# Kernel optimization log

Measured on AMD Instinct MI355X. Metric: run time of the kernel, lower is better.

## Reference

```python
import jax, jax.numpy as jnp
import numpy as np

N_AGENTS = 32
STATE_DIM = 512
EMBED = 64
BATCH = 32768


def setup_inputs() -> dict:
    key = jax.random.key(0)
    ks = jax.random.split(key, 16)
    g = lambda k, shape, fan_in: jax.random.normal(k, shape, jnp.float32) / np.sqrt(fan_in)
    return {
        "agent_qs": jax.random.normal(ks[0], (BATCH, N_AGENTS), jnp.float32),
        "states": jax.random.normal(ks[1], (BATCH, STATE_DIM), jnp.float32),
        # hyper_w1: Linear(state,E) -> ReLU -> Linear(E, n_agents*E)
        "w1_l1_w": g(ks[2], (EMBED, STATE_DIM), STATE_DIM),
        "w1_l1_b": jnp.zeros((EMBED,), jnp.float32),
        "w1_l2_w": g(ks[3], (N_AGENTS * EMBED, EMBED), EMBED),
        "w1_l2_b": jnp.zeros((N_AGENTS * EMBED,), jnp.float32),
        # hyper_w2: Linear(state,E) -> ReLU -> Linear(E, E)
        "w2_l1_w": g(ks[4], (EMBED, STATE_DIM), STATE_DIM),
        "w2_l1_b": jnp.zeros((EMBED,), jnp.float32),
        "w2_l2_w": g(ks[5], (EMBED, EMBED), EMBED),
        "w2_l2_b": jnp.zeros((EMBED,), jnp.float32),
        # hyper_b1: Linear(state, E)
        "b1_w": g(ks[6], (EMBED, STATE_DIM), STATE_DIM),
        "b1_b": jnp.zeros((EMBED,), jnp.float32),
        # hyper_b2: Linear(state,E) -> ReLU -> Linear(E, 1)
        "b2_l1_w": g(ks[7], (EMBED, STATE_DIM), STATE_DIM),
        "b2_l1_b": jnp.zeros((EMBED,), jnp.float32),
        "b2_l2_w": g(ks[8], (1, EMBED), EMBED),
        "b2_l2_b": jnp.zeros((1,), jnp.float32),
    }


def _linear(x, w, b):
    return x @ w.T + b


def reference(agent_qs, states,
              w1_l1_w, w1_l1_b, w1_l2_w, w1_l2_b,
              w2_l1_w, w2_l1_b, w2_l2_w, w2_l2_b,
              b1_w, b1_b, b2_l1_w, b2_l1_b, b2_l2_w, b2_l2_b):
    B = agent_qs.shape[0]
    # hypernetworks producing per-sample weights
    w1 = jnp.abs(_linear(jax.nn.relu(_linear(states, w1_l1_w, w1_l1_b)), w1_l2_w, w1_l2_b))
    w1 = w1.reshape(B, N_AGENTS, EMBED)                      # [B, A, E]
    b1 = _linear(states, b1_w, b1_b)                         # [B, E]
    hidden = jax.nn.elu(jnp.einsum('ba,bae->be', agent_qs, w1) + b1)  # [B, E]
    w2 = jnp.abs(_linear(jax.nn.relu(_linear(states, w2_l1_w, w2_l1_b)), w2_l2_w, w2_l2_b))  # [B, E]
    b2 = _linear(jax.nn.relu(_linear(states, b2_l1_w, b2_l1_b)), b2_l2_w, b2_l2_b)           # [B, 1]
    q_total = jnp.einsum('be,be->b', hidden, w2) + b2[:, 0]  # [B]
    return q_total
```

## Files before the change

### kernel.cpp

```cpp
#include <hip/hip_runtime.h>

typedef unsigned short u16;
typedef unsigned int u32;
typedef short bf16x8 __attribute__((ext_vector_type(8)));
typedef float f32x4 __attribute__((ext_vector_type(4)));

#define NAG 32
#define STATE 512
#define EMBED 64
#define TB 32

#define OFF_W1L1 0
#define OFF_W2L1 32768
#define OFF_B1W  65536
#define OFF_B2L1 98304
#define OFF_W1L2 131072
#define OFF_W2L2 262144
#define WS_TOTAL 266240

__device__ __forceinline__ float bf2f(u16 u) {
    u32 i = ((u32)u) << 16; float f;
    __builtin_memcpy(&f, &i, 4); return f;
}
__device__ __forceinline__ u16 f2bf(float f) {
    u32 i; __builtin_memcpy(&i, &f, 4);
    return (u16)((i + 0x8000u) >> 16);
}
__device__ __forceinline__ bf16x8 ld8(const u16* p) {
    return *reinterpret_cast<const bf16x8*>(p);
}
__device__ __forceinline__ bf16x8 cvt8(f32x4 a, f32x4 b) {
    bf16x8 r;
#pragma unroll
    for (int i = 0; i < 4; ++i) r[i]     = (short)f2bf(a[i]);
#pragma unroll
    for (int i = 0; i < 4; ++i) r[i + 4] = (short)f2bf(b[i]);
    return r;
}
__device__ __forceinline__ void dma16(const void* g, void* l) {
    __builtin_amdgcn_global_load_lds(
        (const __attribute__((address_space(1))) u32*)g,
        (__attribute__((address_space(3))) u32*)l, 16, 0, 0);
}

__global__ __launch_bounds__(256) void cvt_weights(
    const float* __restrict__ w1l1w, const float* __restrict__ w2l1w,
    const float* __restrict__ b1w,   const float* __restrict__ b2l1w,
    const float* __restrict__ w1l2w, const float* __restrict__ w2l2w,
    u16* __restrict__ ws)
{
    int idx = blockIdx.x * 256 + threadIdx.x;
    const float* src; int off;
    if      (idx < OFF_W2L1)  { src = w1l1w; off = OFF_W1L1; }
    else if (idx < OFF_B1W)   { src = w2l1w; off = OFF_W2L1; }
    else if (idx < OFF_B2L1)  { src = b1w;   off = OFF_B1W;  }
    else if (idx < OFF_W1L2)  { src = b2l1w; off = OFF_B2L1; }
    else if (idx < OFF_W2L2)  { src = w1l2w; off = OFF_W1L2; }
    else if (idx < WS_TOTAL)  { src = w2l2w; off = OFF_W2L2; }
    else return;
    ws[idx] = f2bf(src[idx - off]);
}

__global__ __launch_bounds__(256, 2) void qmix_kernel(
    const float* __restrict__ qs,    const float* __restrict__ st,
    const u16*  __restrict__ wsb,
    const float* __restrict__ w1l1b, const float* __restrict__ w1l2b,
    const float* __restrict__ w2l1b, const float* __restrict__ w2l2b,
    const float* __restrict__ b1b,   const float* __restrict__ b2l1b,
    const float* __restrict__ b2l2w, const float* __restrict__ b2l2b,
    float* __restrict__ out)
{
    __shared__ u16   wbuf[256 * 64];
    __shared__ float sbuf[TB * 64];
    __shared__ u16   y[TB][264];
    __shared__ u16   hid[TB][72];
    __shared__ float qsl[TB][33];
    __shared__ float w1b[2048];
    __shared__ float qacc[TB][2];
    __shared__ float b2w[64];

    const int t    = threadIdx.x;
    const int wave = t >> 6, lane = t & 63;
    const int m = lane & 15, quad = lane >> 4;
    const int sbase = blockIdx.x * TB;

    if (t < 64) b2w[t] = b2l2w[t];
    {
        int s = t >> 3, a8 = (t & 7) * 4;
        f32x4 qv = *reinterpret_cast<const f32x4*>(qs + (size_t)(sbase + s) * NAG + a8);
#pragma unroll
        for (int j = 0; j < 4; ++j) qsl[s][a8 + j] = qv[j];
    }
    {
        f32x4 a0 = *reinterpret_cast<const f32x4*>(w1l2b + t * 8);
        f32x4 a1 = *reinterpret_cast<const f32x4*>(w1l2b + t * 8 + 4);
        *reinterpret_cast<f32x4*>(&w1b[t * 8])     = a0;
        *reinterpret_cast<f32x4*>(&w1b[t * 8 + 4]) = a1;
    }

    const int shalf = wave >> 1, fhalf = wave & 1;
    const int s0 = shalf * 16;
    const int fbase = fhalf * 128;

    const float* bgA = fhalf ? b1b   : w1l1b;
    const float* bgB = fhalf ? b2l1b : w2l1b;
    float abias[8];
#pragma unroll
    for (int tt = 0; tt < 4; ++tt) abias[tt]     = bgA[tt * 16 + m];
#pragma unroll
    for (int tt = 0; tt < 4; ++tt) abias[tt + 4] = bgB[tt * 16 + m];

    f32x4 acc[8] = {};
    for (int ksl = 0; ksl < 8; ++ksl) {
        __syncthreads();
        {
            const int rsub = lane >> 3, c = lane & 7;
#pragma unroll
            for (int j = 0; j < 8; ++j) {
                const int row = wave * 64 + j * 8 + rsub;
                const int sc  = c ^ (row & 7);
                dma16(wsb + (size_t)row * STATE + ksl * 64 + sc * 8,
                      &wbuf[(wave * 64 + j * 8) * 64 + lane * 8]);
            }
        }
        {
            const int rs = lane >> 4, cs = lane & 15;
#pragma unroll
            for (int j = 0; j < 2; ++j) {
                const int row = wave * 8 + j * 4 + rs;
                const int sc  = cs ^ (row & 15);
                dma16(st + (size_t)(sbase + row) * STATE + ksl * 64 + sc * 4,
                      &sbuf[(wave * 8 + j * 4) * 64 + lane * 4]);
            }
        }
        __builtin_amdgcn_s_waitcnt(0);
        __syncthreads();
#pragma unroll
        for (int ks = 0; ks < 2; ++ks) {
            const int arow = s0 + m;
            const int gc = ks * 8 + quad * 2;
            f32x4 a0 = *reinterpret_cast<const f32x4*>(&sbuf[arow * 64 + ((gc    ) ^ (arow & 15)) * 4]);
            f32x4 a1 = *reinterpret_cast<const f32x4*>(&sbuf[arow * 64 + ((gc + 1) ^ (arow & 15)) * 4]);
            bf16x8 af = cvt8(a0, a1);
#pragma unroll
            for (int tt = 0; tt < 8; ++tt) {
                const int brow = fbase + tt * 16 + m;
                bf16x8 bf = ld8(&wbuf[brow * 64 + ((ks * 4 + quad) ^ (brow & 7)) * 8]);
                acc[tt] = __builtin_amdgcn_mfma_f32_16x16x32_bf16(af, bf, acc[tt], 0, 0, 0);
            }
        }
    }
#pragma unroll
    for (int tt = 0; tt < 8; ++tt) {
        const bool isrelu = (fhalf == 0) || (tt >= 4);
        const int fcol = fbase + tt * 16 + m;
#pragma unroll
        for (int r = 0; r < 4; ++r) {
            float v = acc[tt][r] + abias[tt];
            if (isrelu) v = fmaxf(v, 0.f);
            y[s0 + quad * 4 + r][fcol] = f2bf(v);
        }
    }
    __syncthreads();

    const int e0 = (wave & 1) * 32;
    bf16x8 haf0 = *reinterpret_cast<const bf16x8*>(&y[s0 + m][quad * 8]);
    bf16x8 haf1 = *reinterpret_cast<const bf16x8*>(&y[s0 + m][32 + quad * 8]);

    f32x4 hacc[2] = {};
    for (int bs = 0; bs < 8; ++bs) {
        {
            const int rsub = lane >> 3, c = lane & 7;
#pragma unroll
            for (int j = 0; j < 8; ++j) {
                const int row = wave * 64 + j * 8 + rsub;
                const int sc  = c ^ (row & 7);
                dma16(wsb + OFF_W1L2 + ((size_t)bs * 256 + row) * EMBED + sc * 8,
                      &wbuf[(wave * 64 + j * 8) * 64 + lane * 8]);
            }
        }
        __builtin_amdgcn_s_waitcnt(0);
        __syncthreads();
#pragma unroll
        for (int aloc = 0; aloc < 4; ++aloc) {
            const int a = bs * 4 + aloc;
            float qv[4];
#pragma unroll
            for (int r = 0; r < 4; ++r) qv[r] = qsl[s0 + quad * 4 + r][a];
#pragma unroll
            for (int tp = 0; tp < 2; ++tp) {
                const int row = aloc * 64 + e0 + tp * 16 + m;
                bf16x8 b0 = ld8(&wbuf[row * 64 + ((    quad) ^ (row & 7)) * 8]);
                bf16x8 b1 = ld8(&wbuf[row * 64 + ((4 + quad) ^ (row & 7)) * 8]);
                f32x4 p = {};
                p = __builtin_amdgcn_mfma_f32_16x16x32_bf16(haf0, b0, p, 0, 0, 0);
                p = __builtin_amdgcn_mfma_f32_16x16x32_bf16(haf1, b1, p, 0, 0, 0);
                float bias = w1b[a * EMBED + e0 + tp * 16 + m];
#pragma unroll
                for (int r = 0; r < 4; ++r)
                    hacc[tp][r] += qv[r] * fabsf(p[r] + bias);
            }
        }
        __syncthreads();
    }
#pragma unroll
    for (int tp = 0; tp < 2; ++tp) {
#pragma unroll
        for (int r = 0; r < 4; ++r) {
            int s = s0 + quad * 4 + r, e = e0 + tp * 16 + m;
            float v = hacc[tp][r] + bf2f(y[s][128 + e]);
            v = (v > 0.f) ? v : (__expf(v) - 1.f);
            hid[s][e] = f2bf(v);
        }
    }
    __syncthreads();

    bf16x8 h2f0 = *reinterpret_cast<const bf16x8*>(&y[s0 + m][64 + quad * 8]);
    bf16x8 h2f1 = *reinterpret_cast<const bf16x8*>(&y[s0 + m][64 + 32 + quad * 8]);

    const u16* wc0 = wsb + OFF_W2L2 + (size_t)((wave & 1) * 32 + m) * EMBED + quad * 8;
    f32x4 qp = {};
#pragma unroll
    for (int tp = 0; tp < 2; ++tp) {
        const int etile = (wave & 1) * 2 + tp;
        bf16x8 b0 = ld8(wc0 + tp * 1024);
        bf16x8 b1 = ld8(wc0 + tp * 1024 + 32);
        f32x4 p = {};
        p = __builtin_amdgcn_mfma_f32_16x16x32_bf16(h2f0, b0, p, 0, 0, 0);
        p = __builtin_amdgcn_mfma_f32_16x16x32_bf16(h2f1, b1, p, 0, 0, 0);
        float bias = w2l2b[etile * 16 + m];
#pragma unroll
        for (int r = 0; r < 4; ++r) {
            float w2v = fabsf(p[r] + bias);
            float hv = bf2f(hid[s0 + quad * 4 + r][etile * 16 + m]);
            qp[r] += hv * w2v;
        }
    }
#pragma unroll
    for (int off = 1; off < 16; off <<= 1) {
#pragma unroll
        for (int r = 0; r < 4; ++r) qp[r] += __shfl_xor(qp[r], off, 64);
    }
    if (m == 0) {
#pragma unroll
        for (int r = 0; r < 4; ++r) qacc[s0 + quad * 4 + r][wave & 1] = qp[r];
    }
    __syncthreads();

    if (t < TB) {
        int s = t;
        float q = qacc[s][0] + qacc[s][1] + b2l2b[0];
        float acc2 = 0.f;
#pragma unroll
        for (int kk = 0; kk < 8; ++kk) {
            bf16x8 hv = *reinterpret_cast<const bf16x8*>(&y[s][192 + kk * 8]);
#pragma unroll
            for (int j = 0; j < 8; ++j)
                acc2 += bf2f((u16)hv[j]) * b2w[kk * 8 + j];
        }
        out[sbase + s] = q + acc2;
    }
}

extern "C" void kernel_launch(void* const* d_in, const int* in_sizes, int n_in,
                              void* d_out, int out_size, void* d_ws, size_t ws_size,
                              hipStream_t stream)
{
    const float* qs    = (const float*)d_in[0];
    const float* st    = (const float*)d_in[1];
    const float* w1l1w = (const float*)d_in[2];
    const float* w1l1b = (const float*)d_in[3];
    const float* w1l2w = (const float*)d_in[4];
    const float* w1l2b = (const float*)d_in[5];
    const float* w2l1w = (const float*)d_in[6];
    const float* w2l1b = (const float*)d_in[7];
    const float* w2l2w = (const float*)d_in[8];
    const float* w2l2b = (const float*)d_in[9];
    const float* b1w   = (const float*)d_in[10];
    const float* b1b   = (const float*)d_in[11];
    const float* b2l1w = (const float*)d_in[12];
    const float* b2l1b = (const float*)d_in[13];
    const float* b2l2w = (const float*)d_in[14];
    const float* b2l2b = (const float*)d_in[15];

    u16* wsb = (u16*)d_ws;

    cvt_weights<<<(WS_TOTAL + 255) / 256, 256, 0, stream>>>(
        w1l1w, w2l1w, b1w, b2l1w, w1l2w, w2l2w, wsb);

    int B = in_sizes[0] / NAG;
    int grid = B / TB;
    qmix_kernel<<<grid, 256, 0, stream>>>(
        qs, st, wsb,
        w1l1b, w1l2b, w2l1b, w2l2b, b1b, b2l1b, b2l2w, b2l2b,
        (float*)d_out);
}
```

Before: 156.3 us.

## Double samples per block so each wave owns 16 samples across all features

Raises the per-block sample tile from 32 to 64. Each wave now computes all 256 first-layer features for its own 16 samples, so each streamed weight slice is reused across twice as many samples. States are loaded straight from global into registers instead of staged through shared memory, and agent Qs and the w1 bias are kept in shared memory as bf16. The hidden buffer now reuses the weight buffer. This halves weight traffic per sample and shrinks shared memory, at the cost of many more accumulator registers per thread (16 f32x4) and less occupancy headroom, plus extra bf16 rounding of qs and the bias.

```diff
diff --git a/kernel.cpp b/kernel.cpp
--- a/kernel.cpp
+++ b/kernel.cpp
@@ -4,11 +4,12 @@
 typedef unsigned int u32;
 typedef short bf16x8 __attribute__((ext_vector_type(8)));
 typedef float f32x4 __attribute__((ext_vector_type(4)));
+typedef u16 u16x4 __attribute__((ext_vector_type(4)));
 
 #define NAG 32
 #define STATE 512
 #define EMBED 64
-#define TB 32
+#define TB 64
 
 #define OFF_W1L1 0
 #define OFF_W2L1 32768
@@ -70,90 +71,77 @@
     const float* __restrict__ b2l2w, const float* __restrict__ b2l2b,
     float* __restrict__ out)
 {
-    __shared__ u16   wbuf[256 * 64];
-    __shared__ float sbuf[TB * 64];
-    __shared__ u16   y[TB][264];
-    __shared__ u16   hid[TB][72];
-    __shared__ float qsl[TB][33];
-    __shared__ float w1b[2048];
-    __shared__ float qacc[TB][2];
-    __shared__ float b2w[64];
+    __shared__ u16  wbuf[256 * 64];
+    __shared__ u16  y[TB][264];
+    __shared__ u16  qslb[TB][40];
+    __shared__ u16  w1bs[2048];
+    __shared__ float qacc[TB];
+    __shared__ float b2wv[64];
 
     const int t    = threadIdx.x;
     const int wave = t >> 6, lane = t & 63;
     const int m = lane & 15, quad = lane >> 4;
     const int sbase = blockIdx.x * TB;
-
-    if (t < 64) b2w[t] = b2l2w[t];
+    const int s0 = wave * 16;
+
+    if (t < 64) b2wv[t] = b2l2w[t];
     {
-        int s = t >> 3, a8 = (t & 7) * 4;
-        f32x4 qv = *reinterpret_cast<const f32x4*>(qs + (size_t)(sbase + s) * NAG + a8);
-#pragma unroll
-        for (int j = 0; j < 4; ++j) qsl[s][a8 + j] = qv[j];
-    }
-    {
-        f32x4 a0 = *reinterpret_cast<const f32x4*>(w1l2b + t * 8);
-        f32x4 a1 = *reinterpret_cast<const f32x4*>(w1l2b + t * 8 + 4);
-        *reinterpret_cast<f32x4*>(&w1b[t * 8])     = a0;
-        *reinterpret_cast<f32x4*>(&w1b[t * 8 + 4]) = a1;
-    }
-
-    const int shalf = wave >> 1, fhalf = wave & 1;
-    const int s0 = shalf * 16;
-    const int fbase = fhalf * 128;
-
-    const float* bgA = fhalf ? b1b   : w1l1b;
-    const float* bgB = fhalf ? b2l1b : w2l1b;
-    float abias[8];
-#pragma unroll
-    for (int tt = 0; tt < 4; ++tt) abias[tt]     = bgA[tt * 16 + m];
-#pragma unroll
-    for (int tt = 0; tt < 4; ++tt) abias[tt + 4] = bgB[tt * 16 + m];
-
-    f32x4 acc[8] = {};
+        f32x4 q0 = *reinterpret_cast<const f32x4*>(qs + (size_t)sbase * NAG + t * 8);
+        f32x4 q1 = *reinterpret_cast<const f32x4*>(qs + (size_t)sbase * NAG + t * 8 + 4);
+        *reinterpret_cast<bf16x8*>(&qslb[t >> 2][(t & 3) * 8]) = cvt8(q0, q1);
+        f32x4 w0 = *reinterpret_cast<const f32x4*>(w1l2b + t * 8);
+        f32x4 w1 = *reinterpret_cast<const f32x4*>(w1l2b + t * 8 + 4);
+        *reinterpret_cast<bf16x8*>(&w1bs[t * 8]) = cvt8(w0, w1);
+    }
+
+    float abias[16];
+#pragma unroll
+    for (int tt = 0; tt < 4; ++tt) abias[tt]      = w1l1b[tt * 16 + m];
+#pragma unroll
+    for (int tt = 0; tt < 4; ++tt) abias[tt + 4]  = w2l1b[tt * 16 + m];
+#pragma unroll
+    for (int tt = 0; tt < 4; ++tt) abias[tt + 8]  = b1b[tt * 16 + m];
+#pragma unroll
+    for (int tt = 0; tt < 4; ++tt) abias[tt + 12] = b2l1b[tt * 16 + m];
+
+    const float* astB = st + (size_t)(sbase + s0 + m) * STATE + quad * 8;
+    const int rsub = lane >> 3, cch = lane & 7;
+
+    f32x4 acc[16] = {};
     for (int ksl = 0; ksl < 8; ++ksl) {
         __syncthreads();
-        {
-            const int rsub = lane >> 3, c = lane & 7;
-#pragma unroll
-            for (int j = 0; j < 8; ++j) {
-                const int row = wave * 64 + j * 8 + rsub;
-                const int sc  = c ^ (row & 7);
-                dma16(wsb + (size_t)row * STATE + ksl * 64 + sc * 8,
-                      &wbuf[(wave * 64 + j * 8) * 64 + lane * 8]);
-            }
-        }
-        {
-            const int rs = lane >> 4, cs = lane & 15;
-#pragma unroll
-            for (int j = 0; j < 2; ++j) {
-                const int row = wave * 8 + j * 4 + rs;
-                const int sc  = cs ^ (row & 15);
-                dma16(st + (size_t)(sbase + row) * STATE + ksl * 64 + sc * 4,
-                      &sbuf[(wave * 8 + j * 4) * 64 + lane * 4]);
-            }
-        }
+#pragma unroll
+        for (int j = 0; j < 8; ++j) {
+            const int row = wave * 64 + j * 8 + rsub;
+            const int sc  = cch ^ (row & 7);
+            dma16(wsb + (size_t)row * STATE + ksl * 64 + sc * 8,
+                  &wbuf[(wave * 64 + j * 8) * 64 + lane * 8]);
+        }
+        f32x4 av0 = *reinterpret_cast<const f32x4*>(astB + ksl * 64);
+        f32x4 av1 = *reinterpret_cast<const f32x4*>(astB + ksl * 64 + 4);
+        f32x4 av2 = *reinterpret_cast<const f32x4*>(astB + ksl * 64 + 32);
+        f32x4 av3 = *reinterpret_cast<const f32x4*>(astB + ksl * 64 + 36);
         __builtin_amdgcn_s_waitcnt(0);
         __syncthreads();
-#pragma unroll
-        for (int ks = 0; ks < 2; ++ks) {
-            const int arow = s0 + m;
-            const int gc = ks * 8 + quad * 2;
-            f32x4 a0 = *reinterpret_cast<const f32x4*>(&sbuf[arow * 64 + ((gc    ) ^ (arow & 15)) * 4]);
-            f32x4 a1 = *reinterpret_cast<const f32x4*>(&sbuf[arow * 64 + ((gc + 1) ^ (arow & 15)) * 4]);
-            bf16x8 af = cvt8(a0, a1);
-#pragma unroll
-            for (int tt = 0; tt < 8; ++tt) {
-                const int brow = fbase + tt * 16 + m;
-                bf16x8 bf = ld8(&wbuf[brow * 64 + ((ks * 4 + quad) ^ (brow & 7)) * 8]);
-                acc[tt] = __builtin_amdgcn_mfma_f32_16x16x32_bf16(af, bf, acc[tt], 0, 0, 0);
-            }
-        }
-    }
-#pragma unroll
-    for (int tt = 0; tt < 8; ++tt) {
-        const bool isrelu = (fhalf == 0) || (tt >= 4);
-        const int fcol = fbase + tt * 16 + m;
+        bf16x8 af0 = cvt8(av0, av1);
+        bf16x8 af1 = cvt8(av2, av3);
+#pragma unroll
+        for (int tt = 0; tt < 16; ++tt) {
+            const int brow = tt * 16 + m;
+            bf16x8 b0 = ld8(&wbuf[brow * 64 + ((quad) ^ (brow & 7)) * 8]);
+            acc[tt] = __builtin_amdgcn_mfma_f32_16x16x32_bf16(af0, b0, acc[tt], 0, 0, 0);
+        }
+#pragma unroll
+        for (int tt = 0; tt < 16; ++tt) {
+            const int brow = tt * 16 + m;
+            bf16x8 b1 = ld8(&wbuf[brow * 64 + ((4 + quad) ^ (brow & 7)) * 8]);
+            acc[tt] = __builtin_amdgcn_mfma_f32_16x16x32_bf16(af1, b1, acc[tt], 0, 0, 0);
+        }
+    }
+#pragma unroll
+    for (int tt = 0; tt < 16; ++tt) {
+        const bool isrelu = (tt < 8) || (tt >= 12);
+        const int fcol = tt * 16 + m;
 #pragma unroll
         for (int r = 0; r < 4; ++r) {
             float v = acc[tt][r] + abias[tt];
@@ -163,78 +151,72 @@
     }
     __syncthreads();
 
-    const int e0 = (wave & 1) * 32;
     bf16x8 haf0 = *reinterpret_cast<const bf16x8*>(&y[s0 + m][quad * 8]);
     bf16x8 haf1 = *reinterpret_cast<const bf16x8*>(&y[s0 + m][32 + quad * 8]);
 
-    f32x4 hacc[2] = {};
+    f32x4 hacc[4] = {};
     for (int bs = 0; bs < 8; ++bs) {
-        {
-            const int rsub = lane >> 3, c = lane & 7;
-#pragma unroll
-            for (int j = 0; j < 8; ++j) {
-                const int row = wave * 64 + j * 8 + rsub;
-                const int sc  = c ^ (row & 7);
-                dma16(wsb + OFF_W1L2 + ((size_t)bs * 256 + row) * EMBED + sc * 8,
-                      &wbuf[(wave * 64 + j * 8) * 64 + lane * 8]);
-            }
-        }
+        __syncthreads();
+#pragma unroll
+        for (int j = 0; j < 8; ++j) {
+            const int row = wave * 64 + j * 8 + rsub;
+            const int sc  = cch ^ (row & 7);
+            dma16(wsb + OFF_W1L2 + ((size_t)bs * 256 + row) * EMBED + sc * 8,
+                  &wbuf[(wave * 64 + j * 8) * 64 + lane * 8]);
+        }
+        u16x4 qv4[4];
+#pragma unroll
+        for (int r = 0; r < 4; ++r)
+            qv4[r] = *reinterpret_cast<const u16x4*>(&qslb[s0 + quad * 4 + r][bs * 4]);
         __builtin_amdgcn_s_waitcnt(0);
         __syncthreads();
 #pragma unroll
         for (int aloc = 0; aloc < 4; ++aloc) {
-            const int a = bs * 4 + aloc;
-            float qv[4];
-#pragma unroll
-            for (int r = 0; r < 4; ++r) qv[r] = qsl[s0 + quad * 4 + r][a];
-#pragma unroll
-            for (int tp = 0; tp < 2; ++tp) {
-                const int row = aloc * 64 + e0 + tp * 16 + m;
-                bf16x8 b0 = ld8(&wbuf[row * 64 + ((    quad) ^ (row & 7)) * 8]);
+#pragma unroll
+            for (int tp = 0; tp < 4; ++tp) {
+                const int row = aloc * 64 + tp * 16 + m;
+                bf16x8 b0 = ld8(&wbuf[row * 64 + ((quad) ^ (row & 7)) * 8]);
                 bf16x8 b1 = ld8(&wbuf[row * 64 + ((4 + quad) ^ (row & 7)) * 8]);
                 f32x4 p = {};
                 p = __builtin_amdgcn_mfma_f32_16x16x32_bf16(haf0, b0, p, 0, 0, 0);
                 p = __builtin_amdgcn_mfma_f32_16x16x32_bf16(haf1, b1, p, 0, 0, 0);
-                float bias = w1b[a * EMBED + e0 + tp * 16 + m];
+                const float bias = bf2f(w1bs[(bs * 4 + aloc) * EMBED + tp * 16 + m]);
 #pragma unroll
                 for (int r = 0; r < 4; ++r)
-                    hacc[tp][r] += qv[r] * fabsf(p[r] + bias);
+                    hacc[tp][r] += bf2f((u16)qv4[r][aloc]) * fabsf(p[r] + bias);
             }
         }
-        __syncthreads();
-    }
-#pragma unroll
-    for (int tp = 0; tp < 2; ++tp) {
+    }
+    __syncthreads();
+    u16* hid = wbuf;
+#pragma unroll
+    for (int tp = 0; tp < 4; ++tp) {
 #pragma unroll
         for (int r = 0; r < 4; ++r) {
-            int s = s0 + quad * 4 + r, e = e0 + tp * 16 + m;
+            const int s = s0 + quad * 4 + r, e = tp * 16 + m;
             float v = hacc[tp][r] + bf2f(y[s][128 + e]);
             v = (v > 0.f) ? v : (__expf(v) - 1.f);
-            hid[s][e] = f2bf(v);
+            hid[s * 66 + e] = f2bf(v);
         }
     }
     __syncthreads();
 
     bf16x8 h2f0 = *reinterpret_cast<const bf16x8*>(&y[s0 + m][64 + quad * 8]);
-    bf16x8 h2f1 = *reinterpret_cast<const bf16x8*>(&y[s0 + m][64 + 32 + quad * 8]);
-
-    const u16* wc0 = wsb + OFF_W2L2 + (size_t)((wave & 1) * 32 + m) * EMBED + quad * 8;
+    bf16x8 h2f1 = *reinterpret_cast<const bf16x8*>(&y[s0 + m][96 + quad * 8]);
+
     f32x4 qp = {};
 #pragma unroll
-    for (int tp = 0; tp < 2; ++tp) {
-        const int etile = (wave & 1) * 2 + tp;
-        bf16x8 b0 = ld8(wc0 + tp * 1024);
-        bf16x8 b1 = ld8(wc0 + tp * 1024 + 32);
+    for (int tp = 0; tp < 4; ++tp) {
+        const u16* wc = wsb + OFF_W2L2 + (size_t)(tp * 16 + m) * EMBED + quad * 8;
+        bf16x8 b0 = ld8(wc);
+        bf16x8 b1 = ld8(wc + 32);
         f32x4 p = {};
         p = __builtin_amdgcn_mfma_f32_16x16x32_bf16(h2f0, b0, p, 0, 0, 0);
         p = __builtin_amdgcn_mfma_f32_16x16x32_bf16(h2f1, b1, p, 0, 0, 0);
-        float bias = w2l2b[etile * 16 + m];
-#pragma unroll
-        for (int r = 0; r < 4; ++r) {
-            float w2v = fabsf(p[r] + bias);
-            float hv = bf2f(hid[s0 + quad * 4 + r][etile * 16 + m]);
-            qp[r] += hv * w2v;
-        }
+        const float bias = w2l2b[tp * 16 + m];
+#pragma unroll
+        for (int r = 0; r < 4; ++r)
+            qp[r] += bf2f(hid[(s0 + quad * 4 + r) * 66 + tp * 16 + m]) * fabsf(p[r] + bias);
     }
 #pragma unroll
     for (int off = 1; off < 16; off <<= 1) {
@@ -243,22 +225,21 @@
     }
     if (m == 0) {
 #pragma unroll
-        for (int r = 0; r < 4; ++r) qacc[s0 + quad * 4 + r][wave & 1] = qp[r];
+        for (int r = 0; r < 4; ++r) qacc[s0 + quad * 4 + r] = qp[r];
     }
     __syncthreads();
 
     if (t < TB) {
-        int s = t;
-        float q = qacc[s][0] + qacc[s][1] + b2l2b[0];
+        float q = qacc[t] + b2l2b[0];
         float acc2 = 0.f;
 #pragma unroll
         for (int kk = 0; kk < 8; ++kk) {
-            bf16x8 hv = *reinterpret_cast<const bf16x8*>(&y[s][192 + kk * 8]);
+            bf16x8 hv = *reinterpret_cast<const bf16x8*>(&y[t][192 + kk * 8]);
 #pragma unroll
             for (int j = 0; j < 8; ++j)
-                acc2 += bf2f((u16)hv[j]) * b2w[kk * 8 + j];
-        }
-        out[sbase + s] = q + acc2;
+                acc2 += bf2f((u16)hv[j]) * b2wv[kk * 8 + j];
+        }
+        out[sbase + t] = q + acc2;
     }
 }
 
```

Result: faster. 152.1 us (-2.7%).
